# Kernel optimization log

Hardware: AMD Instinct MI355X
Metric: run time of the kernel (lower is better)

The kernel has to match this reference:

```python
import jax, jax.numpy as jnp
import numpy as np

OUT, IN = 4096, 4096
GROUP_SIZE = 64
NUM_GROUPS = IN // GROUP_SIZE  # 64


def dequantize(packed, mn, scale):
    # packed: [OUT, NUM_GROUPS, GROUP_SIZE//2] int32, byte values 0..255.
    # 4-bit asymmetric layout (torch compress): high nibble holds the first
    # half of each group, low nibble the second half.
    hi = (packed >> 4) & 0xF                      # [OUT, G, 32]
    lo = packed & 0xF                             # [OUT, G, 32]
    vals = jnp.concatenate([hi, lo], axis=-1).astype(jnp.float32)  # [OUT, G, 64]
    w = vals / scale + mn                         # scale, mn broadcast [OUT, G, 1]
    return w.reshape(OUT, IN)


def setup_inputs() -> dict:
    key = jax.random.key(0)
    k1, k2, k3, k4, k5 = jax.random.split(key, 5)
    x = jax.random.normal(k1, (4, 2048, IN), dtype=jnp.float32)
    packed = jax.random.randint(k2, (OUT, NUM_GROUPS, GROUP_SIZE // 2), 0, 256, dtype=jnp.int32)
    mn = jax.random.normal(k3, (OUT, NUM_GROUPS, 1), dtype=jnp.float32) * 0.02
    # scale = B / (mx - mn) is positive; keep it away from zero.
    scale = jax.random.uniform(k4, (OUT, NUM_GROUPS, 1), dtype=jnp.float32) * 200.0 + 100.0
    bias = jax.random.normal(k5, (OUT,), dtype=jnp.float32) * 0.02
    return {"x": x, "packed": packed, "mn": mn, "scale": scale, "bias": bias}


def reference(x, packed, mn, scale, bias):
    w = dequantize(packed, mn, scale)             # [OUT, IN] fp32
    # F.linear: out = x @ w.T + bias
    return jnp.einsum('bsk,nk->bsn', x, w) + bias
```

## Files before the change

### kernel.cpp

```cpp
#include <hip/hip_runtime.h>

typedef unsigned short u16;
typedef unsigned int u32;
typedef _Float16 f16;
typedef f16 f16x2 __attribute__((ext_vector_type(2)));
typedef f16 f16x8 __attribute__((ext_vector_type(8)));
typedef __fp16 h16x2 __attribute__((ext_vector_type(2)));
typedef float f32x4 __attribute__((ext_vector_type(4)));

#define M_DIM 8192
#define N_DIM 4096
#define K_DIM 4096

#define XCVT_BLOCKS 16384
#define W4_BLOCKS 8192
#define IM_BLOCKS 1024

__global__ __launch_bounds__(256) void prep_kernel(
    const float4* __restrict__ x, uint4* __restrict__ xh,
    const int* __restrict__ packed, u32* __restrict__ w4,
    const float* __restrict__ mn, const float* __restrict__ scale,
    uint2* __restrict__ invmn) {
  int b = blockIdx.x;
  if (b < XCVT_BLOCKS) {
    uint2* xh2 = (uint2*)xh;
    int i0 = b * 512 + threadIdx.x;
    float4 a0 = x[i0];
    float4 a1 = x[i0 + 256];
    h16x2 h0 = __builtin_amdgcn_cvt_pkrtz(a0.x, a0.y);
    h16x2 h1 = __builtin_amdgcn_cvt_pkrtz(a0.z, a0.w);
    h16x2 h2 = __builtin_amdgcn_cvt_pkrtz(a1.x, a1.y);
    h16x2 h3 = __builtin_amdgcn_cvt_pkrtz(a1.z, a1.w);
    uint2 o0, o1;
    o0.x = __builtin_bit_cast(u32, h0);
    o0.y = __builtin_bit_cast(u32, h1);
    o1.x = __builtin_bit_cast(u32, h2);
    o1.y = __builtin_bit_cast(u32, h3);
    xh2[i0] = o0;
    xh2[i0 + 256] = o1;
  } else if (b < XCVT_BLOCKS + W4_BLOCKS) {
    int idx = (b - XCVT_BLOCKS) * 256 + threadIdx.x;
    int n = idx >> 9, w = idx & 511;
    int g = w >> 3;
    int jb = (w & 7) << 3;
    int sh = (jb < 32) ? 4 : 0;
    const int* p = packed + n * 2048 + g * 32 + (jb & 31);
    u32 out = 0;
#pragma unroll
    for (int t = 0; t < 8; t++) {
      u32 nib = ((u32)p[t] >> sh) & 0xFu;
      int pos = ((t & 1) ? 16 : 0) + ((t >> 1) << 2);
      out |= nib << pos;
    }
    w4[idx] = out;
  } else {
    int idx = (b - XCVT_BLOCKS - W4_BLOCKS) * 256 + threadIdx.x;
    int n = idx & 4095, g = idx >> 12;
    float sc = scale[n * 64 + g];
    float m = mn[n * 64 + g];
    f16 invh = (f16)(1.0f / sc);
    f16 mnh = (f16)(m - 16.0f * (float)invh);
    u32 ib = (u32)__builtin_bit_cast(u16, invh);
    u32 mb = (u32)__builtin_bit_cast(u16, mnh);
    uint2 o;
    o.x = ib | (ib << 16);
    o.y = mb | (mb << 16);
    invmn[idx] = o;
  }
}

__device__ __forceinline__ void gload_lds16(const void* g, void* l) {
  __builtin_amdgcn_global_load_lds(
      (const __attribute__((address_space(1))) void*)g,
      (__attribute__((address_space(3))) void*)l, 16, 0, 0);
}

__global__ __launch_bounds__(256, 2) void gemm4_kernel(
    const u16* __restrict__ A,
    const u32* __restrict__ B4,
    const uint2* __restrict__ IM,
    const float* __restrict__ bias, float* __restrict__ C) {
  __shared__ alignas(16) u16 As[2][256 * 32];
  __shared__ alignas(16) u32 Bs[2][128 * 4];

  const int tid = threadIdx.x;
  const int wave = tid >> 6, lane = tid & 63;
  const int lr = lane & 15, lq = lane >> 4;
  const int wg = ((int)blockIdx.x & 7) * 128 + ((int)blockIdx.x >> 3);
  const int bn = wg & 31, bm = wg >> 5;
  const int m0 = bm << 8, n0 = bn << 7;
  const int wm = (wave & 1) << 7, wn = (wave >> 1) << 6;

  const int chunkg = (lane & 3) ^ ((lane >> 3) & 3);
  const u16* pA =
      A + (size_t)(m0 + (wave << 6) + (lane >> 2)) * K_DIM + (chunkg << 3);
  char* dstA = (char*)(&As[0][0]) + wave * 4096 + lane * 16;
  const u32* pB = B4 + (size_t)(n0 + ((wave & 1) << 6) + lane) * 512 +
                  ((wave >> 1) << 2);
  char* dstB = (char*)(&Bs[0][0]) + wave * 1024 + lane * 16;
  const uint2* pI = IM + n0 + wn + lr;
  const int aswz = (lq ^ ((lr >> 1) & 3)) << 4;

  f32x4 acc[8][4] = {};

  for (int kk = 0; kk < 64; ++kk) {
    uint2 im[4];
    const uint2* pIt = pI + kk * 4096;
#pragma unroll
    for (int j = 0; j < 4; j++) im[j] = pIt[j * 16];

#pragma unroll
    for (int s = 0; s < 2; s++)
#pragma unroll
      for (int c = 0; c < 4; c++)
        gload_lds16(pA + kk * 64 + s * 32 + (size_t)c * 16 * K_DIM,
                    dstA + s * 16384 + c * 1024);
    gload_lds16(pB + kk * 8, dstB);
    __syncthreads();

#pragma unroll
    for (int s = 0; s < 2; s++) {
      f16x8 af[8];
#pragma unroll
      for (int i = 0; i < 8; i++)
        af[i] = *(const f16x8*)((const char*)(&As[0][0]) + s * 16384 +
                                (wm + i * 16 + lr) * 64 + aswz);
      u32 braw[4];
#pragma unroll
      for (int j = 0; j < 4; j++) braw[j] = Bs[s][(wn + j * 16 + lr) * 4 + lq];

      f16x8 bf[4];
#pragma unroll
      for (int j = 0; j < 4; j++) {
        u32 d = braw[j];
        u32 q0 = ((d << 6) & 0x03C003C0u) | 0x4C004C00u;
        u32 q1 = ((d << 2) & 0x03C003C0u) | 0x4C004C00u;
        u32 q2 = ((d >> 2) & 0x03C003C0u) | 0x4C004C00u;
        u32 q3 = ((d >> 6) & 0x03C003C0u) | 0x4C004C00u;
        f16x2 inv2 = __builtin_bit_cast(f16x2, im[j].x);
        f16x2 mn2 = __builtin_bit_cast(f16x2, im[j].y);
        f16x2 w0 = __builtin_elementwise_fma(__builtin_bit_cast(f16x2, q0), inv2, mn2);
        f16x2 w1 = __builtin_elementwise_fma(__builtin_bit_cast(f16x2, q1), inv2, mn2);
        f16x2 w2 = __builtin_elementwise_fma(__builtin_bit_cast(f16x2, q2), inv2, mn2);
        f16x2 w3 = __builtin_elementwise_fma(__builtin_bit_cast(f16x2, q3), inv2, mn2);
        union {
          f16x8 v;
          u32 d[4];
        } u;
        u.d[0] = __builtin_bit_cast(u32, w0);
        u.d[1] = __builtin_bit_cast(u32, w1);
        u.d[2] = __builtin_bit_cast(u32, w2);
        u.d[3] = __builtin_bit_cast(u32, w3);
        bf[j] = u.v;
      }
#pragma unroll
      for (int i = 0; i < 8; i++)
#pragma unroll
        for (int j = 0; j < 4; j++)
          acc[i][j] = __builtin_amdgcn_mfma_f32_16x16x32_f16(af[i], bf[j],
                                                             acc[i][j], 0, 0, 0);
    }
    __syncthreads();
  }

#pragma unroll
  for (int j = 0; j < 4; j++) {
    int n = n0 + wn + j * 16 + lr;
    float bv = bias[n];
#pragma unroll
    for (int i = 0; i < 8; i++) {
      int mb = m0 + wm + i * 16 + (lq << 2);
#pragma unroll
      for (int t = 0; t < 4; t++)
        C[(size_t)(mb + t) * N_DIM + n] = acc[i][j][t] + bv;
    }
  }
}

__global__ __launch_bounds__(256) void fallback_gemm(
    const float* __restrict__ x, const int* __restrict__ packed,
    const float* __restrict__ mn, const float* __restrict__ scale,
    const float* __restrict__ bias, float* __restrict__ out) {
  __shared__ float As[16][17];
  __shared__ float Bs[16][17];
  int tx = threadIdx.x & 15, ty = threadIdx.x >> 4;
  int m = blockIdx.y * 16 + ty;
  int n = blockIdx.x * 16 + tx;
  float acc = 0.f;
  for (int k0 = 0; k0 < K_DIM; k0 += 16) {
    As[ty][tx] = x[(size_t)m * K_DIM + k0 + tx];
    int nn = blockIdx.x * 16 + ty;
    int k = k0 + tx;
    int g = k >> 6, pos = k & 63;
    int p = packed[nn * 2048 + g * 32 + (pos & 31)];
    int v = (pos < 32) ? ((p >> 4) & 0xF) : (p & 0xF);
    Bs[ty][tx] = (float)v / scale[nn * 64 + g] + mn[nn * 64 + g];
    __syncthreads();
#pragma unroll
    for (int kk = 0; kk < 16; kk++) acc += As[ty][kk] * Bs[tx][kk];
    __syncthreads();
  }
  out[(size_t)m * N_DIM + n] = acc + bias[n];
}

extern "C" void kernel_launch(void* const* d_in, const int* in_sizes, int n_in,
                              void* d_out, int out_size, void* d_ws,
                              size_t ws_size, hipStream_t stream) {
  const float* x = (const float*)d_in[0];
  const int* packed = (const int*)d_in[1];
  const float* mn = (const float*)d_in[2];
  const float* scale = (const float*)d_in[3];
  const float* bias = (const float*)d_in[4];
  float* out = (float*)d_out;

  const size_t offW4 = (size_t)M_DIM * K_DIM * 2;
  const size_t offIM = offW4 + (size_t)N_DIM * K_DIM / 2;
  const size_t need = offIM + (size_t)64 * N_DIM * 8;

  if (ws_size >= need) {
    u16* Xh = (u16*)d_ws;
    u32* W4 = (u32*)((char*)d_ws + offW4);
    uint2* IMp = (uint2*)((char*)d_ws + offIM);
    prep_kernel<<<XCVT_BLOCKS + W4_BLOCKS + IM_BLOCKS, 256, 0, stream>>>(
        (const float4*)x, (uint4*)Xh, packed, W4, mn, scale, IMp);
    gemm4_kernel<<<(M_DIM / 256) * (N_DIM / 128), 256, 0, stream>>>(
        Xh, W4, IMp, bias, out);
  } else {
    dim3 grid(N_DIM / 16, M_DIM / 16);
    fallback_gemm<<<grid, 256, 0, stream>>>(x, packed, mn, scale, bias, out);
  }
}
```

Measured before the change: 531.8 us.

## Dequantize weights to fp16 in prep and use a 4-stage pipelined 256x256 GEMM

The prep kernel now fully dequantizes the 4-bit weights into an fp16 matrix, so the GEMM no longer unpacks nibbles in its inner loop and runs a plain fp16 x fp16 MFMA GEMM. The GEMM moves to 256x256 tiles with 512 threads and a 4-deep LDS ring buffer filled by direct global-to-LDS loads. It uses explicit vmcnt waits, barriers and setprio to overlap loads with MFMA work. In exchange, weight traffic grows (fp16 instead of packed 4-bit) and LDS use per block rises, which may reduce occupancy.

Result: no change. 537.0 us (+1.0%).

```diff
diff --git a/kernel.cpp b/kernel.cpp
--- a/kernel.cpp
+++ b/kernel.cpp
@@ -13,17 +13,14 @@
 #define K_DIM 4096
 
 #define XCVT_BLOCKS 16384
-#define W4_BLOCKS 8192
-#define IM_BLOCKS 1024
+#define BH_BLOCKS 8192
 
 __global__ __launch_bounds__(256) void prep_kernel(
-    const float4* __restrict__ x, uint4* __restrict__ xh,
-    const int* __restrict__ packed, u32* __restrict__ w4,
-    const float* __restrict__ mn, const float* __restrict__ scale,
-    uint2* __restrict__ invmn) {
+    const float4* __restrict__ x, uint2* __restrict__ xh,
+    const int* __restrict__ packed, const float* __restrict__ mn,
+    const float* __restrict__ scale, uint4* __restrict__ bh) {
   int b = blockIdx.x;
   if (b < XCVT_BLOCKS) {
-    uint2* xh2 = (uint2*)xh;
     int i0 = b * 512 + threadIdx.x;
     float4 a0 = x[i0];
     float4 a1 = x[i0 + 256];
@@ -36,36 +33,39 @@
     o0.y = __builtin_bit_cast(u32, h1);
     o1.x = __builtin_bit_cast(u32, h2);
     o1.y = __builtin_bit_cast(u32, h3);
-    xh2[i0] = o0;
-    xh2[i0 + 256] = o1;
-  } else if (b < XCVT_BLOCKS + W4_BLOCKS) {
+    xh[i0] = o0;
+    xh[i0 + 256] = o1;
+  } else {
     int idx = (b - XCVT_BLOCKS) * 256 + threadIdx.x;
     int n = idx >> 9, w = idx & 511;
     int g = w >> 3;
-    int jb = (w & 7) << 3;
-    int sh = (jb < 32) ? 4 : 0;
-    const int* p = packed + n * 2048 + g * 32 + (jb & 31);
-    u32 out = 0;
-#pragma unroll
-    for (int t = 0; t < 8; t++) {
-      u32 nib = ((u32)p[t] >> sh) & 0xFu;
-      int pos = ((t & 1) ? 16 : 0) + ((t >> 1) << 2);
-      out |= nib << pos;
-    }
-    w4[idx] = out;
-  } else {
-    int idx = (b - XCVT_BLOCKS - W4_BLOCKS) * 256 + threadIdx.x;
-    int n = idx & 4095, g = idx >> 12;
+    int sh = ((w & 7) < 4) ? 4 : 0;
+    const int* p = packed + n * 2048 + g * 32 + (w & 3) * 8;
     float sc = scale[n * 64 + g];
     float m = mn[n * 64 + g];
     f16 invh = (f16)(1.0f / sc);
     f16 mnh = (f16)(m - 16.0f * (float)invh);
-    u32 ib = (u32)__builtin_bit_cast(u16, invh);
-    u32 mb = (u32)__builtin_bit_cast(u16, mnh);
-    uint2 o;
-    o.x = ib | (ib << 16);
-    o.y = mb | (mb << 16);
-    invmn[idx] = o;
+    f16x2 inv2, mn2;
+    inv2[0] = invh;
+    inv2[1] = invh;
+    mn2[0] = mnh;
+    mn2[1] = mnh;
+    union {
+      f16x8 v;
+      uint4 d;
+    } o;
+#pragma unroll
+    for (int u = 0; u < 4; u++) {
+      u32 v0 = ((u32)p[2 * u] >> sh) & 0xFu;
+      u32 v1 = ((u32)p[2 * u + 1] >> sh) & 0xFu;
+      f16x2 q;
+      q[0] = (f16)(int)(16 + v0);
+      q[1] = (f16)(int)(16 + v1);
+      f16x2 wv = __builtin_elementwise_fma(q, inv2, mn2);
+      o.v[2 * u] = wv[0];
+      o.v[2 * u + 1] = wv[1];
+    }
+    bh[idx] = o.d;
   }
 }
 
@@ -75,93 +75,103 @@
       (__attribute__((address_space(3))) void*)l, 16, 0, 0);
 }
 
-__global__ __launch_bounds__(256, 2) void gemm4_kernel(
+__global__ __launch_bounds__(512, 2) void gemm4_kernel(
     const u16* __restrict__ A,
-    const u32* __restrict__ B4,
-    const uint2* __restrict__ IM,
+    const u16* __restrict__ Bh,
     const float* __restrict__ bias, float* __restrict__ C) {
-  __shared__ alignas(16) u16 As[2][256 * 32];
-  __shared__ alignas(16) u32 Bs[2][128 * 4];
+  __shared__ alignas(16) u16 AS[4][256 * 32];
+  __shared__ alignas(16) u16 BS[4][256 * 32];
 
   const int tid = threadIdx.x;
   const int wave = tid >> 6, lane = tid & 63;
   const int lr = lane & 15, lq = lane >> 4;
-  const int wg = ((int)blockIdx.x & 7) * 128 + ((int)blockIdx.x >> 3);
-  const int bn = wg & 31, bm = wg >> 5;
-  const int m0 = bm << 8, n0 = bn << 7;
+  const int wg = ((int)blockIdx.x & 7) * 64 + ((int)blockIdx.x >> 3);
+  const int bn = wg & 15, bm = wg >> 4;
+  const int m0 = bm << 8, n0 = bn << 8;
   const int wm = (wave & 1) << 7, wn = (wave >> 1) << 6;
 
-  const int chunkg = (lane & 3) ^ ((lane >> 3) & 3);
-  const u16* pA =
-      A + (size_t)(m0 + (wave << 6) + (lane >> 2)) * K_DIM + (chunkg << 3);
-  char* dstA = (char*)(&As[0][0]) + wave * 4096 + lane * 16;
-  const u32* pB = B4 + (size_t)(n0 + ((wave & 1) << 6) + lane) * 512 +
-                  ((wave >> 1) << 2);
-  char* dstB = (char*)(&Bs[0][0]) + wave * 1024 + lane * 16;
-  const uint2* pI = IM + n0 + wn + lr;
-  const int aswz = (lq ^ ((lr >> 1) & 3)) << 4;
+  const int csA = ((lane & 3) ^ ((lane >> 3) & 3)) << 3;
+  const u16* pA0 = A + (size_t)(m0 + (wave << 5) + (lane >> 2)) * K_DIM + csA;
+  const u16* pA1 = pA0 + (size_t)16 * K_DIM;
+  const u16* pB0 = Bh + (size_t)(n0 + (wave << 5) + (lane >> 2)) * K_DIM + csA;
+  const u16* pB1 = pB0 + (size_t)16 * K_DIM;
+  char* dA = (char*)(&AS[0][0]) + (wave << 11) + (lane << 4);
+  char* dB = (char*)(&BS[0][0]) + (wave << 11) + (lane << 4);
+
+  const int swz = (lq ^ ((lr >> 1) & 3)) << 4;
+  const int aoff = (wm + lr) * 64 + swz;
+  const int boff = (wn + lr) * 64 + swz;
+
+#define STAGEU(hh, u)                                                    \
+  do {                                                                   \
+    gload_lds16(((u) ? pA1 : pA0) + (hh) * 32,                           \
+                dA + (((hh) & 3) << 14) + ((u) << 10));                  \
+    gload_lds16(((u) ? pB1 : pB0) + (hh) * 32,                           \
+                dB + (((hh) & 3) << 14) + ((u) << 10));                  \
+  } while (0)
 
   f32x4 acc[8][4] = {};
 
-  for (int kk = 0; kk < 64; ++kk) {
-    uint2 im[4];
-    const uint2* pIt = pI + kk * 4096;
-#pragma unroll
-    for (int j = 0; j < 4; j++) im[j] = pIt[j * 16];
-
-#pragma unroll
-    for (int s = 0; s < 2; s++)
-#pragma unroll
-      for (int c = 0; c < 4; c++)
-        gload_lds16(pA + kk * 64 + s * 32 + (size_t)c * 16 * K_DIM,
-                    dstA + s * 16384 + c * 1024);
-    gload_lds16(pB + kk * 8, dstB);
-    __syncthreads();
-
-#pragma unroll
-    for (int s = 0; s < 2; s++) {
-      f16x8 af[8];
-#pragma unroll
-      for (int i = 0; i < 8; i++)
-        af[i] = *(const f16x8*)((const char*)(&As[0][0]) + s * 16384 +
-                                (wm + i * 16 + lr) * 64 + aswz);
-      u32 braw[4];
-#pragma unroll
-      for (int j = 0; j < 4; j++) braw[j] = Bs[s][(wn + j * 16 + lr) * 4 + lq];
-
-      f16x8 bf[4];
-#pragma unroll
-      for (int j = 0; j < 4; j++) {
-        u32 d = braw[j];
-        u32 q0 = ((d << 6) & 0x03C003C0u) | 0x4C004C00u;
-        u32 q1 = ((d << 2) & 0x03C003C0u) | 0x4C004C00u;
-        u32 q2 = ((d >> 2) & 0x03C003C0u) | 0x4C004C00u;
-        u32 q3 = ((d >> 6) & 0x03C003C0u) | 0x4C004C00u;
-        f16x2 inv2 = __builtin_bit_cast(f16x2, im[j].x);
-        f16x2 mn2 = __builtin_bit_cast(f16x2, im[j].y);
-        f16x2 w0 = __builtin_elementwise_fma(__builtin_bit_cast(f16x2, q0), inv2, mn2);
-        f16x2 w1 = __builtin_elementwise_fma(__builtin_bit_cast(f16x2, q1), inv2, mn2);
-        f16x2 w2 = __builtin_elementwise_fma(__builtin_bit_cast(f16x2, q2), inv2, mn2);
-        f16x2 w3 = __builtin_elementwise_fma(__builtin_bit_cast(f16x2, q3), inv2, mn2);
-        union {
-          f16x8 v;
-          u32 d[4];
-        } u;
-        u.d[0] = __builtin_bit_cast(u32, w0);
-        u.d[1] = __builtin_bit_cast(u32, w1);
-        u.d[2] = __builtin_bit_cast(u32, w2);
-        u.d[3] = __builtin_bit_cast(u32, w3);
-        bf[j] = u.v;
-      }
-#pragma unroll
-      for (int i = 0; i < 8; i++)
-#pragma unroll
-        for (int j = 0; j < 4; j++)
-          acc[i][j] = __builtin_amdgcn_mfma_f32_16x16x32_f16(af[i], bf[j],
-                                                             acc[i][j], 0, 0, 0);
-    }
-    __syncthreads();
-  }
+  STAGEU(0, 0);
+  STAGEU(0, 1);
+  STAGEU(1, 0);
+  STAGEU(1, 1);
+  STAGEU(2, 0);
+  STAGEU(2, 1);
+  asm volatile("s_waitcnt vmcnt(8)" ::: "memory");
+  __builtin_amdgcn_s_barrier();
+
+#pragma unroll 1
+  for (int h = 0; h < 128; ++h) {
+    const char* aS = (const char*)(&AS[0][0]) + ((h & 3) << 14);
+    const char* bS = (const char*)(&BS[0][0]) + ((h & 3) << 14);
+
+    f16x8 af[4], bf[4];
+#pragma unroll
+    for (int i = 0; i < 4; i++)
+      af[i] = *(const f16x8*)(aS + aoff + i * 1024);
+#pragma unroll
+    for (int j = 0; j < 4; j++)
+      bf[j] = *(const f16x8*)(bS + boff + j * 1024);
+    if (h <= 124) STAGEU(h + 3, 0);
+    __builtin_amdgcn_s_barrier();
+    asm volatile("s_waitcnt lgkmcnt(0)" ::: "memory");
+    __builtin_amdgcn_sched_barrier(0);
+    __builtin_amdgcn_s_setprio(1);
+#pragma unroll
+    for (int i = 0; i < 4; i++)
+#pragma unroll
+      for (int j = 0; j < 4; j++)
+        acc[i][j] = __builtin_amdgcn_mfma_f32_16x16x32_f16(af[i], bf[j],
+                                                           acc[i][j], 0, 0, 0);
+    __builtin_amdgcn_s_setprio(0);
+    __builtin_amdgcn_s_barrier();
+
+    f16x8 ag[4];
+#pragma unroll
+    for (int i = 0; i < 4; i++)
+      ag[i] = *(const f16x8*)(aS + aoff + (4 + i) * 1024);
+    if (h <= 124) STAGEU(h + 3, 1);
+    if (h <= 124)
+      asm volatile("s_waitcnt vmcnt(8)" ::: "memory");
+    else if (h == 125)
+      asm volatile("s_waitcnt vmcnt(4)" ::: "memory");
+    else if (h == 126)
+      asm volatile("s_waitcnt vmcnt(0)" ::: "memory");
+    __builtin_amdgcn_s_barrier();
+    asm volatile("s_waitcnt lgkmcnt(0)" ::: "memory");
+    __builtin_amdgcn_sched_barrier(0);
+    __builtin_amdgcn_s_setprio(1);
+#pragma unroll
+    for (int i = 0; i < 4; i++)
+#pragma unroll
+      for (int j = 0; j < 4; j++)
+        acc[4 + i][j] = __builtin_amdgcn_mfma_f32_16x16x32_f16(
+            ag[i], bf[j], acc[4 + i][j], 0, 0, 0);
+    __builtin_amdgcn_s_setprio(0);
+    __builtin_amdgcn_s_barrier();
+  }
+#undef STAGEU
 
 #pragma unroll
   for (int j = 0; j < 4; j++) {
@@ -213,18 +223,16 @@
   const float* bias = (const float*)d_in[4];
   float* out = (float*)d_out;
 
-  const size_t offW4 = (size_t)M_DIM * K_DIM * 2;
-  const size_t offIM = offW4 + (size_t)N_DIM * K_DIM / 2;
-  const size_t need = offIM + (size_t)64 * N_DIM * 8;
+  const size_t offBh = (size_t)M_DIM * K_DIM * 2;
+  const size_t need = offBh + (size_t)N_DIM * K_DIM * 2;
 
   if (ws_size >= need) {
     u16* Xh = (u16*)d_ws;
-    u32* W4 = (u32*)((char*)d_ws + offW4);
-    uint2* IMp = (uint2*)((char*)d_ws + offIM);
-    prep_kernel<<<XCVT_BLOCKS + W4_BLOCKS + IM_BLOCKS, 256, 0, stream>>>(
-        (const float4*)x, (uint4*)Xh, packed, W4, mn, scale, IMp);
-    gemm4_kernel<<<(M_DIM / 256) * (N_DIM / 128), 256, 0, stream>>>(
-        Xh, W4, IMp, bias, out);
+    u16* Bhp = (u16*)((char*)d_ws + offBh);
+    prep_kernel<<<XCVT_BLOCKS + BH_BLOCKS, 256, 0, stream>>>(
+        (const float4*)x, (uint2*)Xh, packed, mn, scale, (uint4*)Bhp);
+    gemm4_kernel<<<(M_DIM / 256) * (N_DIM / 256), 512, 0, stream>>>(
+        Xh, Bhp, bias, out);
   } else {
     dim3 grid(N_DIM / 16, M_DIM / 16);
     fallback_gemm<<<grid, 256, 0, stream>>>(x, packed, mn, scale, bias, out);
```
